# Kernel tuning notes

Measured on AMD Instinct MI355X. Metric: run time of the kernel, lower is better.

## Reference

```python
import jax, jax.numpy as jnp
import numpy as np

EPS = 1e-6


def _mp_cos_pointwise(p, q, M2):
    # p, q: [B, L, K]; M2: [C, K] (squared perspective weights)
    # cosine between (p*M_c) and (q*M_c) along K, per channel c -> [B, L, C]
    num = jnp.einsum('blk,blk,ck->blc', p, q, M2)
    pn = jnp.sqrt(jnp.maximum(jnp.einsum('blk,ck->blc', p * p, M2), EPS))
    qn = jnp.sqrt(jnp.maximum(jnp.einsum('blk,ck->blc', q * q, M2), EPS))
    return num / pn / qn


def setup_inputs() -> dict:
    key = jax.random.key(0)
    ks = jax.random.split(key, 10)
    B, Lq, Ld, K, C = 32, 200, 200, 200, 50
    f32 = jnp.float32
    def unif(k, shape):  # keras 'uniform' init: U(-0.05, 0.05)
        return jax.random.uniform(k, shape, f32, -0.05, 0.05)
    return {
        'q_rep': jax.random.normal(ks[0], (B, Lq, K), f32),
        'q_last': jax.random.normal(ks[1], (B, K), f32),
        'q_mask': jnp.ones((B, Lq), f32),
        'd_rep': jax.random.normal(ks[2], (B, Ld, K), f32),
        'd_last': jax.random.normal(ks[3], (B, K), f32),
        'd_mask': jnp.ones((B, Ld), f32),
        'full_M': unif(ks[4], (C, K)),
        'maxpool_M': unif(ks[5], (C, K)),
        'att_M': unif(ks[6], (C, K)),
        'max_att_M': unif(ks[7], (C, K)),
    }


def reference(q_rep, q_last, q_mask, d_rep, d_last, d_mask,
              full_M, maxpool_M, att_M, max_att_M):
    outputs = []

    # relevancy matrix: cosine(q[b,j,:], d[b,i,:]) -> [B, Ld, Lq]
    num = jnp.einsum('bik,bjk->bij', d_rep, q_rep)
    dn = jnp.sqrt(jnp.maximum(jnp.sum(d_rep * d_rep, -1), EPS))  # [B, Ld]
    qn = jnp.sqrt(jnp.maximum(jnp.sum(q_rep * q_rep, -1), EPS))  # [B, Lq]
    rel = num / qn[:, None, :] / dn[:, :, None]
    rel = rel * q_mask[:, None, :] * d_mask[:, :, None]

    # full matching: cosine(d[b,i]*M_c, q_last[b]*M_c) -> [B, Ld, C]
    M2 = full_M * full_M
    fnum = jnp.einsum('bik,bk,ck->bic', d_rep, q_last, M2)
    fpn = jnp.sqrt(jnp.maximum(jnp.einsum('bik,ck->bic', d_rep * d_rep, M2), EPS))
    fqn = jnp.sqrt(jnp.maximum(jnp.einsum('bk,ck->bc', q_last * q_last, M2), EPS))
    outputs.append(fnum / fpn / fqn[:, None, :])

    # maxpool matching: cosine(d[b,i]*M_c, q[b,j]*M_c) -> [B, Ld, Lq, C]
    M2 = maxpool_M * maxpool_M
    mnum = jnp.einsum('bik,bjk,ck->bijc', d_rep, q_rep, M2)
    mpn = jnp.sqrt(jnp.maximum(jnp.einsum('bik,ck->bic', d_rep * d_rep, M2), EPS))
    mqn = jnp.sqrt(jnp.maximum(jnp.einsum('bjk,ck->bjc', q_rep * q_rep, M2), EPS))
    mm = mnum / mpn[:, :, None, :] / mqn[:, None, :, :]
    outputs.append(jnp.concatenate([jnp.max(mm, axis=2), jnp.mean(mm, axis=2)], axis=2))

    # attentive matching: cosine-weighted q rep (no softmax -> normalize by sum)
    wq = jnp.einsum('bij,bjk->bik', rel, q_rep)
    wq = wq / (jnp.sum(rel, axis=-1) + EPS)[..., None]  # [B, Ld, K]
    outputs.append(_mp_cos_pointwise(d_rep, wq, att_M * att_M))

    # max-attentive matching: gather best-matching q word per d position
    idx = jnp.argmax(rel, axis=2)  # [B, Ld]
    max_q = jnp.take_along_axis(q_rep, idx[:, :, None], axis=1)  # [B, Ld, K]
    outputs.append(_mp_cos_pointwise(d_rep, max_q, max_att_M * max_att_M))

    return jnp.concatenate(outputs, axis=-1)  # [B, Ld, 5*C]
```

## Files before the change

### kernel.cpp

```cpp
#include <hip/hip_runtime.h>
#include <math.h>


#define EPS 1e-6f
#define NEG_HUGE -3.4e38f

typedef __bf16 bf16x8 __attribute__((ext_vector_type(8)));
typedef float f32x16 __attribute__((ext_vector_type(16)));

constexpr size_t OFF_M2ALL = 0;
constexpr size_t OFF_M2B16 = 40000;
constexpr size_t OFF_QB16  = 63296;
constexpr size_t OFF_DB16  = 915264;
constexpr size_t OFF_INVFPN= 1767232;
constexpr size_t OFF_INVMPN= 2087232;
constexpr size_t OFF_INVAPN= 2407232;
constexpr size_t OFF_INVXPN= 2727232;
constexpr size_t OFF_INVMQN= 3047232;
constexpr size_t OFF_INVXQN= 3367232;
constexpr size_t OFF_INVFQN= 3687232;
constexpr size_t OFF_INVDN = 3688832;
constexpr size_t OFF_INVQN = 3695232;
constexpr size_t OFF_IDX   = 3701632;
constexpr size_t OFF_WQ    = 3708032;
constexpr size_t OFF_G     = 4988032;
constexpr size_t OFF_PMAX2 = 6268032;
constexpr size_t OFF_PSUM2 = 6677632;

__global__ __launch_bounds__(256) void k_prep(
    const float* __restrict__ qR, const float* __restrict__ dR,
    const float* __restrict__ fM, const float* __restrict__ mM,
    const float* __restrict__ aM, const float* __restrict__ xM,
    unsigned short* __restrict__ qb16, unsigned short* __restrict__ db16,
    float* __restrict__ invdn, float* __restrict__ invqn,
    float* __restrict__ m2all, unsigned short* __restrict__ m2b16)
{
  int blk = blockIdx.x;
  int tid = threadIdx.x;
  if (blk < 4096) {
    int task = blk*4 + (tid >> 6);
    int l = tid & 63;
    int isQ = task >= 8192;
    int r = isQ ? task - 8192 : task;
    int b = r >> 8, j = r & 255;
    unsigned short* dst = (isQ ? qb16 : db16) + (size_t)r*208;
    if (j < 200) {
      const float* src = (isQ ? qR : dR) + (size_t)(b*200 + j)*200;
      float4 v = {0.f,0.f,0.f,0.f};
      if (l < 50) v = *(const float4*)(src + l*4);
      float s = fmaf(v.x,v.x, fmaf(v.y,v.y, fmaf(v.z,v.z, v.w*v.w)));
#pragma unroll
      for (int m = 32; m; m >>= 1) s += __shfl_xor(s, m);
      if (l == 0) {
        float rr = rsqrtf(fmaxf(s, EPS));
        if (isQ) invqn[b*200 + j] = rr; else invdn[b*200 + j] = rr;
      }
      if (l < 52) {
        ushort4 o = {0,0,0,0};
        if (l < 50) {
          __bf16 h0=(__bf16)v.x, h1=(__bf16)v.y, h2=(__bf16)v.z, h3=(__bf16)v.w;
          o.x = *(unsigned short*)&h0; o.y = *(unsigned short*)&h1;
          o.z = *(unsigned short*)&h2; o.w = *(unsigned short*)&h3;
        }
        *(ushort4*)(dst + l*4) = o;
      }
    } else {
      if (l < 52) { ushort4 z = {0,0,0,0}; *(ushort4*)(dst + l*4) = z; }
    }
  } else {
    int i = (blk - 4096)*256 + tid;
    if (i < 40000) {
      int m = i / 10000, r = i % 10000;
      const float* s = (m==0)?fM:(m==1)?mM:(m==2)?aM:xM;
      float v = s[r];
      m2all[i] = v*v;
    }
    if (i < 224*208) {
      int row = i / 208, k = i % 208;
      unsigned short o = 0;
      if (row < 200 && k < 200) {
        int m = row / 50, c = row % 50;
        const float* s = (m==0)?fM:(m==1)?mM:(m==2)?aM:xM;
        float v = s[c*200 + k];
        __bf16 h = (__bf16)(v*v);
        o = *(unsigned short*)&h;
      }
      m2b16[i] = o;
    }
  }
}

__global__ __launch_bounds__(256,4) void k_gemm1_mfma(
    const float* __restrict__ dR, const float* __restrict__ qR,
    const float* __restrict__ qL, const unsigned short* __restrict__ m2b16,
    float* __restrict__ invfpn, float* __restrict__ invmpn,
    float* __restrict__ invapn, float* __restrict__ invxpn,
    float* __restrict__ invmqn, float* __restrict__ invxqn,
    float* __restrict__ invfqn)
{
  int tid = threadIdx.x;
  int w = tid >> 6, lane = tid & 63;
  int n = lane & 31, h = lane >> 5;
  int task = blockIdx.x*4 + w;
  if (task >= 2807) return;
  int rt = task / 7, nt = task % 7;
  int row = rt*32 + n;

  const float* src;
  if (row < 6400)       src = dR + (size_t)row*200;
  else if (row < 12800) src = qR + (size_t)(row-6400)*200;
  else                  src = qL + (size_t)(row-12800)*200;

  bf16x8 afrag[13];
#pragma unroll
  for (int ks = 0; ks < 13; ks++) {
    int ko = ks*16 + h*8;
    bf16x8 af;
    if (ko < 200) {
      float4 a0 = *(const float4*)(src + ko);
      float4 a1 = *(const float4*)(src + ko + 4);
      af[0] = (__bf16)(a0.x*a0.x); af[1] = (__bf16)(a0.y*a0.y);
      af[2] = (__bf16)(a0.z*a0.z); af[3] = (__bf16)(a0.w*a0.w);
      af[4] = (__bf16)(a1.x*a1.x); af[5] = (__bf16)(a1.y*a1.y);
      af[6] = (__bf16)(a1.z*a1.z); af[7] = (__bf16)(a1.w*a1.w);
    } else {
#pragma unroll
      for (int z = 0; z < 8; z++) af[z] = (__bf16)0.0f;
    }
    afrag[ks] = af;
  }

  f32x16 C;
#pragma unroll
  for (int z = 0; z < 16; z++) C[z] = 0.f;
  const unsigned short* bp = m2b16 + (size_t)(nt*32 + n)*208 + h*8;
#pragma unroll
  for (int ks = 0; ks < 13; ks++) {
    bf16x8 bf = *(const bf16x8*)(bp + ks*16);
    C = __builtin_amdgcn_mfma_f32_32x32x16_bf16(afrag[ks], bf, C, 0, 0, 0);
  }

  int cp = nt*32 + n;
  if (cp < 200) {
    int m = cp / 50, c = cp % 50;
#pragma unroll
    for (int r = 0; r < 16; r++) {
      int grow = rt*32 + (r & 3) + 8*(r >> 2) + 4*h;
      float v = rsqrtf(fmaxf(C[r], EPS));
      if (grow < 6400) {
        if (m == 0)      invfpn[grow*50 + c] = v;
        else if (m == 1) invmpn[grow*50 + c] = v;
        else if (m == 2) invapn[grow*50 + c] = v;
        else             invxpn[grow*50 + c] = v;
      } else if (grow < 12800) {
        int r2 = grow - 6400;
        if (m == 1)      invmqn[c*6400 + r2] = v;
        else if (m == 3) invxqn[r2*50 + c] = v;
      } else {
        if (m == 0)      invfqn[(grow-12800)*50 + c] = v;
      }
    }
  }
}

__global__ __launch_bounds__(256) void k_relwq(
    const float* __restrict__ dR, const float* __restrict__ qR,
    const float* __restrict__ qMask, const float* __restrict__ dMask,
    const float* __restrict__ invdn, const float* __restrict__ invqn,
    float* __restrict__ wq, int* __restrict__ idxout)
{
  __shared__ __align__(16) float qsh[200*68];
  __shared__ float relsh[8][256];
  __shared__ float redv[4][8][2];
  __shared__ int   redi[4][8];
  __shared__ float invrs_sh[8];
  int tid = threadIdx.x;
  int b  = blockIdx.x / 25;
  int i0 = (blockIdx.x % 25) * 8;
  int j = tid, jr = min(j, 199);
  bool jv = j < 200;
  const float* qb = qR + b*40000;
  const float* db = dR + (b*200 + i0)*200;
  float acc[8];
#pragma unroll
  for (int ii = 0; ii < 8; ii++) acc[ii] = 0.f;

  for (int p = 0; p < 4; p++) {
    int kp = p*64; int nk = (p < 3) ? 64 : 8;
    int nch = nk >> 2;
    __syncthreads();
    for (int s = tid; s < 200*nch; s += 256) {
      int jj = s / nch, kk4 = (s - jj*nch)*4;
      float4 v = *(const float4*)(qb + jj*200 + kp + kk4);
      *(float4*)(qsh + jj*68 + kk4) = v;
    }
    __syncthreads();
    for (int k4 = 0; k4 < nk; k4 += 4) {
      float4 qv = *(const float4*)(qsh + jr*68 + k4);
#pragma unroll
      for (int ii = 0; ii < 8; ii++) {
        acc[ii] = fmaf(db[ii*200 + kp + k4 + 0], qv.x, acc[ii]);
        acc[ii] = fmaf(db[ii*200 + kp + k4 + 1], qv.y, acc[ii]);
        acc[ii] = fmaf(db[ii*200 + kp + k4 + 2], qv.z, acc[ii]);
        acc[ii] = fmaf(db[ii*200 + kp + k4 + 3], qv.w, acc[ii]);
      }
    }
  }

  float iqn = invqn[b*200 + jr];
  float qm  = qMask[b*200 + jr];
  int w = tid >> 6, l = tid & 63;
  float rv[8];
#pragma unroll
  for (int ii = 0; ii < 8; ii++) {
    float idn = invdn[b*200 + i0 + ii];
    float dm  = dMask[b*200 + i0 + ii];
    float r = acc[ii]*iqn*idn*qm*dm;
    rv[ii] = r;
    relsh[ii][j] = jv ? r : 0.f;
  }
#pragma unroll
  for (int ii = 0; ii < 8; ii++) {
    float vm = jv ? rv[ii] : NEG_HUGE;
    float vs = jv ? rv[ii] : 0.f;
    int bj = jr;
#pragma unroll
    for (int m = 32; m; m >>= 1) {
      float ov = __shfl_xor(vm, m);
      int   oj = __shfl_xor(bj, m);
      vs += __shfl_xor(vs, m);
      if (ov > vm || (ov == vm && oj < bj)) { vm = ov; bj = oj; }
    }
    if (l == 0) { redv[w][ii][0] = vm; redv[w][ii][1] = vs; redi[w][ii] = bj; }
  }
  __syncthreads();
  if (tid < 8) {
    float bv = redv[0][tid][0], ss = redv[0][tid][1]; int bj = redi[0][tid];
    for (int w2 = 1; w2 < 4; w2++) {
      ss += redv[w2][tid][1];
      float wv = redv[w2][tid][0]; int wj = redi[w2][tid];
      if (wv > bv || (wv == bv && wj < bj)) { bv = wv; bj = wj; }
    }
    invrs_sh[tid] = 1.f/(ss + EPS);
    idxout[b*200 + i0 + tid] = bj;
  }
  __syncthreads();

  int kl = min(tid, 199); bool kv = tid < 200;
  float acw[8];
#pragma unroll
  for (int ii = 0; ii < 8; ii++) acw[ii] = 0.f;
  for (int j0 = 0; j0 < 200; j0 += 4) {
    float qv0 = qb[(j0+0)*200 + kl];
    float qv1 = qb[(j0+1)*200 + kl];
    float qv2 = qb[(j0+2)*200 + kl];
    float qv3 = qb[(j0+3)*200 + kl];
#pragma unroll
    for (int ii = 0; ii < 8; ii++) {
      float4 rs = *(const float4*)&relsh[ii][j0];
      acw[ii] = fmaf(rs.x, qv0, acw[ii]);
      acw[ii] = fmaf(rs.y, qv1, acw[ii]);
      acw[ii] = fmaf(rs.z, qv2, acw[ii]);
      acw[ii] = fmaf(rs.w, qv3, acw[ii]);
    }
  }
#pragma unroll
  for (int ii = 0; ii < 8; ii++) {
    float v = acw[ii]*invrs_sh[ii];
    if (kv) wq[(size_t)(b*200 + i0 + ii)*200 + tid] = v;
  }
}

__global__ __launch_bounds__(256,4) void k_gemm2_mfma(
    const float* __restrict__ dR, const float* __restrict__ qR,
    const float* __restrict__ qL, const float* __restrict__ wq,
    const int* __restrict__ idx, const unsigned short* __restrict__ m2b16,
    float* __restrict__ G)
{
  int tid = threadIdx.x;
  int w = tid >> 6, lane = tid & 63;
  int n = lane & 31, h = lane >> 5;
  int task = blockIdx.x*4 + w;
  int mp = task / 400;
  int sub = task % 400;
  int rt = sub >> 1, nt = sub & 1;
  int row = rt*32 + n;
  int bb = row / 200;
  int msel = (mp == 0) ? 0 : (mp == 3) ? 3 : 2;

  const float* s0 = dR + (size_t)row*200;
  const float* s1;
  if (mp == 0)      s1 = qL + (size_t)bb*200;
  else if (mp == 1) s1 = wq + (size_t)row*200;
  else if (mp == 2) { s0 = wq + (size_t)row*200; s1 = s0; }
  else              s1 = qR + (size_t)(bb*200 + idx[row])*200;

  bf16x8 afrag[13];
#pragma unroll
  for (int ks = 0; ks < 13; ks++) {
    int ko = ks*16 + h*8;
    bf16x8 af;
    if (ko < 200) {
      float4 a0 = *(const float4*)(s0 + ko);
      float4 a1 = *(const float4*)(s0 + ko + 4);
      float4 b0 = *(const float4*)(s1 + ko);
      float4 b1 = *(const float4*)(s1 + ko + 4);
      af[0] = (__bf16)(a0.x*b0.x); af[1] = (__bf16)(a0.y*b0.y);
      af[2] = (__bf16)(a0.z*b0.z); af[3] = (__bf16)(a0.w*b0.w);
      af[4] = (__bf16)(a1.x*b1.x); af[5] = (__bf16)(a1.y*b1.y);
      af[6] = (__bf16)(a1.z*b1.z); af[7] = (__bf16)(a1.w*b1.w);
    } else {
#pragma unroll
      for (int z = 0; z < 8; z++) af[z] = (__bf16)0.0f;
    }
    afrag[ks] = af;
  }

  f32x16 C;
#pragma unroll
  for (int z = 0; z < 16; z++) C[z] = 0.f;
  const unsigned short* bp = m2b16 + (size_t)(msel*50 + nt*32 + n)*208 + h*8;
#pragma unroll
  for (int ks = 0; ks < 13; ks++) {
    bf16x8 bf = *(const bf16x8*)(bp + ks*16);
    C = __builtin_amdgcn_mfma_f32_32x32x16_bf16(afrag[ks], bf, C, 0, 0, 0);
  }
  int cc = nt*32 + n;
  if (cc < 50) {
#pragma unroll
    for (int r = 0; r < 16; r++) {
      int mrow = (r & 3) + 8*(r >> 2) + 4*h;
      G[(size_t)(mp*6400 + rt*32 + mrow)*50 + cc] = C[r];
    }
  }
}

__global__ __launch_bounds__(512,2) void k_maxpool_mfma(
    const unsigned short* __restrict__ db16, const unsigned short* __restrict__ qb16,
    const float* __restrict__ m2all, const float* __restrict__ invmqn,
    float* __restrict__ pmax2, float* __restrict__ psum2)
{
  __shared__ __align__(16) unsigned short qsh[128*216];
  int tid = threadIdx.x;
  int b = blockIdx.x / 50, c = blockIdx.x % 50;
  int w = tid >> 6, lane = tid & 63;
  int n = lane & 31, h = lane >> 5;
  const float* M2 = m2all + 10000 + c*200;
  const unsigned short* dbp = db16 + (size_t)(b*256 + w*32 + n)*208 + h*8;

  bf16x8 afrag[13];
#pragma unroll
  for (int ks = 0; ks < 13; ks++) afrag[ks] = *(const bf16x8*)(dbp + ks*16);

  float vm[16], vs[16];
#pragma unroll
  for (int r = 0; r < 16; r++) { vm[r] = NEG_HUGE; vs[r] = 0.f; }

  for (int jh = 0; jh < 2; jh++) {
    int nrows = jh ? 96 : 128;
    int njt   = jh ? 3 : 4;
    __syncthreads();
    {
      const unsigned short* src = qb16 + (size_t)(b*256 + jh*128)*208;
      const float* iqb = invmqn + c*6400 + b*200;
      for (int s = tid; s < nrows*26; s += 512) {
        int r = s / 26, ch = s - r*26;
        int j = jh*128 + r;
        float iq = (j < 200) ? iqb[j] : 0.f;
        int k0 = ch*8;
        bf16x8 v = *(const bf16x8*)(src + (size_t)r*208 + k0);
        float4 m0 = *(const float4*)(M2 + k0);
        float4 m1 = *(const float4*)(M2 + k0 + 4);
        bf16x8 o;
        o[0] = (__bf16)((float)v[0]*iq*m0.x); o[1] = (__bf16)((float)v[1]*iq*m0.y);
        o[2] = (__bf16)((float)v[2]*iq*m0.z); o[3] = (__bf16)((float)v[3]*iq*m0.w);
        o[4] = (__bf16)((float)v[4]*iq*m1.x); o[5] = (__bf16)((float)v[5]*iq*m1.y);
        o[6] = (__bf16)((float)v[6]*iq*m1.z); o[7] = (__bf16)((float)v[7]*iq*m1.w);
        *(bf16x8*)(qsh + r*216 + k0) = o;
      }
    }
    __syncthreads();

    for (int jt = 0; jt < njt; jt++) {
      f32x16 C;
#pragma unroll
      for (int z = 0; z < 16; z++) C[z] = 0.f;
      const unsigned short* bptr = qsh + (jt*32 + n)*216 + h*8;
#pragma unroll
      for (int ks = 0; ks < 13; ks++) {
        bf16x8 bf = *(const bf16x8*)(bptr + ks*16);
        C = __builtin_amdgcn_mfma_f32_32x32x16_bf16(afrag[ks], bf, C, 0, 0, 0);
      }
      bool jv = (jh*128 + jt*32 + n) < 200;
#pragma unroll
      for (int r = 0; r < 16; r++) {
        vm[r] = fmaxf(vm[r], jv ? C[r] : NEG_HUGE);
        vs[r] += C[r];
      }
    }
  }

#pragma unroll
  for (int r = 0; r < 16; r++) {
    float a = vm[r], s = vs[r];
#pragma unroll
    for (int m = 1; m <= 16; m <<= 1) {
      a = fmaxf(a, __shfl_xor(a, m));
      s += __shfl_xor(s, m);
    }
    vm[r] = a; vs[r] = s;
  }
  if (n == 0) {
#pragma unroll
    for (int r = 0; r < 16; r++) {
      int i = w*32 + (r & 3) + 8*(r >> 2) + 4*h;
      pmax2[(size_t)blockIdx.x*256 + i] = vm[r];
      psum2[(size_t)blockIdx.x*256 + i] = vs[r];
    }
  }
}

__global__ void k_out(
    const float* __restrict__ G, const float* __restrict__ pmax2,
    const float* __restrict__ psum2, const float* __restrict__ invfpn,
    const float* __restrict__ invmpn, const float* __restrict__ invapn,
    const float* __restrict__ invxpn, const float* __restrict__ invfqn,
    const float* __restrict__ invxqn, const int* __restrict__ idx,
    float* __restrict__ out)
{
  int row = blockIdx.x;
  int l = threadIdx.x;
  if (l >= 250) return;
  int b = row / 200, i = row % 200;
  int seg = l / 50, c = l % 50;
  float o;
  if (seg == 0) {
    o = G[(size_t)(0*6400 + row)*50 + c] * invfpn[row*50 + c] * invfqn[b*50 + c];
  } else if (seg == 1) {
    o = pmax2[(size_t)(b*50 + c)*256 + i] * invmpn[row*50 + c];
  } else if (seg == 2) {
    o = psum2[(size_t)(b*50 + c)*256 + i] * invmpn[row*50 + c] * (1.f/200.f);
  } else if (seg == 3) {
    o = G[(size_t)(1*6400 + row)*50 + c] * invapn[row*50 + c]
        * rsqrtf(fmaxf(G[(size_t)(2*6400 + row)*50 + c], EPS));
  } else {
    int jid = idx[row];
    o = G[(size_t)(3*6400 + row)*50 + c] * invxpn[row*50 + c]
        * invxqn[(b*200 + jid)*50 + c];
  }
  out[(size_t)row*250 + l] = o;
}

extern "C" void kernel_launch(void* const* d_in, const int* in_sizes, int n_in,
                              void* d_out, int out_size, void* d_ws, size_t ws_size,
                              hipStream_t stream) {
  const float* qR = (const float*)d_in[0];
  const float* qL = (const float*)d_in[1];
  const float* qM = (const float*)d_in[2];
  const float* dR = (const float*)d_in[3];
  const float* dM = (const float*)d_in[5];
  const float* fullM = (const float*)d_in[6];
  const float* mpM   = (const float*)d_in[7];
  const float* attM  = (const float*)d_in[8];
  const float* xM    = (const float*)d_in[9];

  float* ws  = (float*)d_ws;
  float* out = (float*)d_out;

  float* m2all  = ws + OFF_M2ALL;
  unsigned short* m2b16 = (unsigned short*)(ws + OFF_M2B16);
  unsigned short* qb16 = (unsigned short*)(ws + OFF_QB16);
  unsigned short* db16 = (unsigned short*)(ws + OFF_DB16);
  float* invfpn = ws + OFF_INVFPN;
  float* invmpn = ws + OFF_INVMPN;
  float* invapn = ws + OFF_INVAPN;
  float* invxpn = ws + OFF_INVXPN;
  float* invmqn = ws + OFF_INVMQN;
  float* invxqn = ws + OFF_INVXQN;
  float* invfqn = ws + OFF_INVFQN;
  float* invdn  = ws + OFF_INVDN;
  float* invqn  = ws + OFF_INVQN;
  int*   idxp   = (int*)(ws + OFF_IDX);
  float* wqp    = ws + OFF_WQ;
  float* G      = ws + OFF_G;
  float* pmax2  = ws + OFF_PMAX2;
  float* psum2  = ws + OFF_PSUM2;

  k_prep<<<4278, 256, 0, stream>>>(qR, dR, fullM, mpM, attM, xM,
                                   qb16, db16, invdn, invqn, m2all, m2b16);
  k_gemm1_mfma<<<702, 256, 0, stream>>>(dR, qR, qL, m2b16,
                                        invfpn, invmpn, invapn, invxpn,
                                        invmqn, invxqn, invfqn);
  k_relwq<<<800, 256, 0, stream>>>(dR, qR, qM, dM, invdn, invqn, wqp, idxp);
  k_gemm2_mfma<<<400, 256, 0, stream>>>(dR, qR, qL, wqp, idxp, m2b16, G);
  k_maxpool_mfma<<<1600, 512, 0, stream>>>(db16, qb16, m2all, invmqn, pmax2, psum2);
  k_out<<<6400, 256, 0, stream>>>(G, pmax2, psum2, invfpn, invmpn, invapn,
                                  invxpn, invfqn, invxqn, idxp, out);
}
```

Baseline: 278.3 us.

## Merge independent kernels into two horizontally fused launches, drop LDS staging in relwq

The norm GEMM and the relevancy/weighted-q kernel become one launch, with blocks dispatched by block index. The maxpool MFMA and the per-row GEMM2 become a second launch. This removes two kernel launches and their tail gaps, and lets independent work overlap on the GPU. The relwq part now reads q rows straight from global memory instead of staging them through shared memory. GEMM2 tasks now run 8 waves per 512-thread block instead of 4 per 256. In exchange, the fused kernels share a launch bound and a register budget, which may lower occupancy for the lighter branch.

```diff
diff --git a/kernel.cpp b/kernel.cpp
--- a/kernel.cpp
+++ b/kernel.cpp
@@ -90,188 +90,178 @@
   }
 }
 
-__global__ __launch_bounds__(256,4) void k_gemm1_mfma(
+__global__ __launch_bounds__(256) void k_mid(
     const float* __restrict__ dR, const float* __restrict__ qR,
     const float* __restrict__ qL, const unsigned short* __restrict__ m2b16,
     float* __restrict__ invfpn, float* __restrict__ invmpn,
     float* __restrict__ invapn, float* __restrict__ invxpn,
     float* __restrict__ invmqn, float* __restrict__ invxqn,
-    float* __restrict__ invfqn)
-{
-  int tid = threadIdx.x;
-  int w = tid >> 6, lane = tid & 63;
-  int n = lane & 31, h = lane >> 5;
-  int task = blockIdx.x*4 + w;
-  if (task >= 2807) return;
-  int rt = task / 7, nt = task % 7;
-  int row = rt*32 + n;
-
-  const float* src;
-  if (row < 6400)       src = dR + (size_t)row*200;
-  else if (row < 12800) src = qR + (size_t)(row-6400)*200;
-  else                  src = qL + (size_t)(row-12800)*200;
-
-  bf16x8 afrag[13];
-#pragma unroll
-  for (int ks = 0; ks < 13; ks++) {
-    int ko = ks*16 + h*8;
-    bf16x8 af;
-    if (ko < 200) {
-      float4 a0 = *(const float4*)(src + ko);
-      float4 a1 = *(const float4*)(src + ko + 4);
-      af[0] = (__bf16)(a0.x*a0.x); af[1] = (__bf16)(a0.y*a0.y);
-      af[2] = (__bf16)(a0.z*a0.z); af[3] = (__bf16)(a0.w*a0.w);
-      af[4] = (__bf16)(a1.x*a1.x); af[5] = (__bf16)(a1.y*a1.y);
-      af[6] = (__bf16)(a1.z*a1.z); af[7] = (__bf16)(a1.w*a1.w);
-    } else {
-#pragma unroll
-      for (int z = 0; z < 8; z++) af[z] = (__bf16)0.0f;
-    }
-    afrag[ks] = af;
-  }
-
-  f32x16 C;
-#pragma unroll
-  for (int z = 0; z < 16; z++) C[z] = 0.f;
-  const unsigned short* bp = m2b16 + (size_t)(nt*32 + n)*208 + h*8;
-#pragma unroll
-  for (int ks = 0; ks < 13; ks++) {
-    bf16x8 bf = *(const bf16x8*)(bp + ks*16);
-    C = __builtin_amdgcn_mfma_f32_32x32x16_bf16(afrag[ks], bf, C, 0, 0, 0);
-  }
-
-  int cp = nt*32 + n;
-  if (cp < 200) {
-    int m = cp / 50, c = cp % 50;
-#pragma unroll
-    for (int r = 0; r < 16; r++) {
-      int grow = rt*32 + (r & 3) + 8*(r >> 2) + 4*h;
-      float v = rsqrtf(fmaxf(C[r], EPS));
-      if (grow < 6400) {
-        if (m == 0)      invfpn[grow*50 + c] = v;
-        else if (m == 1) invmpn[grow*50 + c] = v;
-        else if (m == 2) invapn[grow*50 + c] = v;
-        else             invxpn[grow*50 + c] = v;
-      } else if (grow < 12800) {
-        int r2 = grow - 6400;
-        if (m == 1)      invmqn[c*6400 + r2] = v;
-        else if (m == 3) invxqn[r2*50 + c] = v;
-      } else {
-        if (m == 0)      invfqn[(grow-12800)*50 + c] = v;
-      }
-    }
-  }
-}
-
-__global__ __launch_bounds__(256) void k_relwq(
-    const float* __restrict__ dR, const float* __restrict__ qR,
+    float* __restrict__ invfqn,
     const float* __restrict__ qMask, const float* __restrict__ dMask,
     const float* __restrict__ invdn, const float* __restrict__ invqn,
     float* __restrict__ wq, int* __restrict__ idxout)
 {
-  __shared__ __align__(16) float qsh[200*68];
-  __shared__ float relsh[8][256];
-  __shared__ float redv[4][8][2];
-  __shared__ int   redi[4][8];
-  __shared__ float invrs_sh[8];
   int tid = threadIdx.x;
-  int b  = blockIdx.x / 25;
-  int i0 = (blockIdx.x % 25) * 8;
-  int j = tid, jr = min(j, 199);
-  bool jv = j < 200;
-  const float* qb = qR + b*40000;
-  const float* db = dR + (b*200 + i0)*200;
-  float acc[8];
-#pragma unroll
-  for (int ii = 0; ii < 8; ii++) acc[ii] = 0.f;
-
-  for (int p = 0; p < 4; p++) {
-    int kp = p*64; int nk = (p < 3) ? 64 : 8;
-    int nch = nk >> 2;
+  if (blockIdx.x < 702) {
+    int w = tid >> 6, lane = tid & 63;
+    int n = lane & 31, h = lane >> 5;
+    int task = blockIdx.x*4 + w;
+    if (task >= 2807) return;
+    int rt = task / 7, nt = task % 7;
+    int row = rt*32 + n;
+
+    const float* src;
+    if (row < 6400)       src = dR + (size_t)row*200;
+    else if (row < 12800) src = qR + (size_t)(row-6400)*200;
+    else                  src = qL + (size_t)(row-12800)*200;
+
+    bf16x8 afrag[13];
+#pragma unroll
+    for (int ks = 0; ks < 13; ks++) {
+      int ko = ks*16 + h*8;
+      bf16x8 af;
+      if (ko < 200) {
+        float4 a0 = *(const float4*)(src + ko);
+        float4 a1 = *(const float4*)(src + ko + 4);
+        af[0] = (__bf16)(a0.x*a0.x); af[1] = (__bf16)(a0.y*a0.y);
+        af[2] = (__bf16)(a0.z*a0.z); af[3] = (__bf16)(a0.w*a0.w);
+        af[4] = (__bf16)(a1.x*a1.x); af[5] = (__bf16)(a1.y*a1.y);
+        af[6] = (__bf16)(a1.z*a1.z); af[7] = (__bf16)(a1.w*a1.w);
+      } else {
+#pragma unroll
+        for (int z = 0; z < 8; z++) af[z] = (__bf16)0.0f;
+      }
+      afrag[ks] = af;
+    }
+
+    f32x16 C;
+#pragma unroll
+    for (int z = 0; z < 16; z++) C[z] = 0.f;
+    const unsigned short* bp = m2b16 + (size_t)(nt*32 + n)*208 + h*8;
+#pragma unroll
+    for (int ks = 0; ks < 13; ks++) {
+      bf16x8 bf = *(const bf16x8*)(bp + ks*16);
+      C = __builtin_amdgcn_mfma_f32_32x32x16_bf16(afrag[ks], bf, C, 0, 0, 0);
+    }
+
+    int cp = nt*32 + n;
+    if (cp < 200) {
+      int m = cp / 50, c = cp % 50;
+#pragma unroll
+      for (int r = 0; r < 16; r++) {
+        int grow = rt*32 + (r & 3) + 8*(r >> 2) + 4*h;
+        float v = rsqrtf(fmaxf(C[r], EPS));
+        if (grow < 6400) {
+          if (m == 0)      invfpn[grow*50 + c] = v;
+          else if (m == 1) invmpn[grow*50 + c] = v;
+          else if (m == 2) invapn[grow*50 + c] = v;
+          else             invxpn[grow*50 + c] = v;
+        } else if (grow < 12800) {
+          int r2 = grow - 6400;
+          if (m == 1)      invmqn[c*6400 + r2] = v;
+          else if (m == 3) invxqn[r2*50 + c] = v;
+        } else {
+          if (m == 0)      invfqn[(grow-12800)*50 + c] = v;
+        }
+      }
+    }
+  } else {
+    __shared__ float relsh[8][256];
+    __shared__ float redv[4][8][2];
+    __shared__ int   redi[4][8];
+    __shared__ float invrs_sh[8];
+    int blk = blockIdx.x - 702;
+    int b  = blk / 25;
+    int i0 = (blk % 25) * 8;
+    int j = tid, jr = min(j, 199);
+    bool jv = j < 200;
+    const float* qb = qR + b*40000;
+    const float* db = dR + (b*200 + i0)*200;
+    float acc[8];
+#pragma unroll
+    for (int ii = 0; ii < 8; ii++) acc[ii] = 0.f;
+
+    const float* qrow = qb + jr*200;
+    for (int k4 = 0; k4 < 200; k4 += 4) {
+      float4 qv = *(const float4*)(qrow + k4);
+#pragma unroll
+      for (int ii = 0; ii < 8; ii++) {
+        acc[ii] = fmaf(db[ii*200 + k4 + 0], qv.x, acc[ii]);
+        acc[ii] = fmaf(db[ii*200 + k4 + 1], qv.y, acc[ii]);
+        acc[ii] = fmaf(db[ii*200 + k4 + 2], qv.z, acc[ii]);
+        acc[ii] = fmaf(db[ii*200 + k4 + 3], qv.w, acc[ii]);
+      }
+    }
+
+    float iqn = invqn[b*200 + jr];
+    float qm  = qMask[b*200 + jr];
+    int w = tid >> 6, l = tid & 63;
+    float rv[8];
+#pragma unroll
+    for (int ii = 0; ii < 8; ii++) {
+      float idn = invdn[b*200 + i0 + ii];
+      float dm  = dMask[b*200 + i0 + ii];
+      float r = acc[ii]*iqn*idn*qm*dm;
+      rv[ii] = r;
+      relsh[ii][j] = jv ? r : 0.f;
+    }
+#pragma unroll
+    for (int ii = 0; ii < 8; ii++) {
+      float vm = jv ? rv[ii] : NEG_HUGE;
+      float vs = jv ? rv[ii] : 0.f;
+      int bj = jr;
+#pragma unroll
+      for (int m = 32; m; m >>= 1) {
+        float ov = __shfl_xor(vm, m);
+        int   oj = __shfl_xor(bj, m);
+        vs += __shfl_xor(vs, m);
+        if (ov > vm || (ov == vm && oj < bj)) { vm = ov; bj = oj; }
+      }
+      if (l == 0) { redv[w][ii][0] = vm; redv[w][ii][1] = vs; redi[w][ii] = bj; }
+    }
     __syncthreads();
-    for (int s = tid; s < 200*nch; s += 256) {
-      int jj = s / nch, kk4 = (s - jj*nch)*4;
-      float4 v = *(const float4*)(qb + jj*200 + kp + kk4);
-      *(float4*)(qsh + jj*68 + kk4) = v;
+    if (tid < 8) {
+      float bv = redv[0][tid][0], ss = redv[0][tid][1]; int bj = redi[0][tid];
+      for (int w2 = 1; w2 < 4; w2++) {
+        ss += redv[w2][tid][1];
+        float wv = redv[w2][tid][0]; int wj = redi[w2][tid];
+        if (wv > bv || (wv == bv && wj < bj)) { bv = wv; bj = wj; }
+      }
+      invrs_sh[tid] = 1.f/(ss + EPS);
+      idxout[b*200 + i0 + tid] = bj;
     }
     __syncthreads();
-    for (int k4 = 0; k4 < nk; k4 += 4) {
-      float4 qv = *(const float4*)(qsh + jr*68 + k4);
+
+    int kl = min(tid, 199); bool kv = tid < 200;
+    float acw[8];
+#pragma unroll
+    for (int ii = 0; ii < 8; ii++) acw[ii] = 0.f;
+    for (int j0 = 0; j0 < 200; j0 += 4) {
+      float qv0 = qb[(j0+0)*200 + kl];
+      float qv1 = qb[(j0+1)*200 + kl];
+      float qv2 = qb[(j0+2)*200 + kl];
+      float qv3 = qb[(j0+3)*200 + kl];
 #pragma unroll
       for (int ii = 0; ii < 8; ii++) {
-        acc[ii] = fmaf(db[ii*200 + kp + k4 + 0], qv.x, acc[ii]);
-        acc[ii] = fmaf(db[ii*200 + kp + k4 + 1], qv.y, acc[ii]);
-        acc[ii] = fmaf(db[ii*200 + kp + k4 + 2], qv.z, acc[ii]);
-        acc[ii] = fmaf(db[ii*200 + kp + k4 + 3], qv.w, acc[ii]);
-      }
-    }
-  }
-
-  float iqn = invqn[b*200 + jr];
-  float qm  = qMask[b*200 + jr];
-  int w = tid >> 6, l = tid & 63;
-  float rv[8];
-#pragma unroll
-  for (int ii = 0; ii < 8; ii++) {
-    float idn = invdn[b*200 + i0 + ii];
-    float dm  = dMask[b*200 + i0 + ii];
-    float r = acc[ii]*iqn*idn*qm*dm;
-    rv[ii] = r;
-    relsh[ii][j] = jv ? r : 0.f;
-  }
-#pragma unroll
-  for (int ii = 0; ii < 8; ii++) {
-    float vm = jv ? rv[ii] : NEG_HUGE;
-    float vs = jv ? rv[ii] : 0.f;
-    int bj = jr;
-#pragma unroll
-    for (int m = 32; m; m >>= 1) {
-      float ov = __shfl_xor(vm, m);
-      int   oj = __shfl_xor(bj, m);
-      vs += __shfl_xor(vs, m);
-      if (ov > vm || (ov == vm && oj < bj)) { vm = ov; bj = oj; }
-    }
-    if (l == 0) { redv[w][ii][0] = vm; redv[w][ii][1] = vs; redi[w][ii] = bj; }
-  }
-  __syncthreads();
-  if (tid < 8) {
-    float bv = redv[0][tid][0], ss = redv[0][tid][1]; int bj = redi[0][tid];
-    for (int w2 = 1; w2 < 4; w2++) {
-      ss += redv[w2][tid][1];
-      float wv = redv[w2][tid][0]; int wj = redi[w2][tid];
-      if (wv > bv || (wv == bv && wj < bj)) { bv = wv; bj = wj; }
-    }
-    invrs_sh[tid] = 1.f/(ss + EPS);
-    idxout[b*200 + i0 + tid] = bj;
-  }
-  __syncthreads();
-
-  int kl = min(tid, 199); bool kv = tid < 200;
-  float acw[8];
-#pragma unroll
-  for (int ii = 0; ii < 8; ii++) acw[ii] = 0.f;
-  for (int j0 = 0; j0 < 200; j0 += 4) {
-    float qv0 = qb[(j0+0)*200 + kl];
-    float qv1 = qb[(j0+1)*200 + kl];
-    float qv2 = qb[(j0+2)*200 + kl];
-    float qv3 = qb[(j0+3)*200 + kl];
+        float4 rs = *(const float4*)&relsh[ii][j0];
+        acw[ii] = fmaf(rs.x, qv0, acw[ii]);
+        acw[ii] = fmaf(rs.y, qv1, acw[ii]);
+        acw[ii] = fmaf(rs.z, qv2, acw[ii]);
+        acw[ii] = fmaf(rs.w, qv3, acw[ii]);
+      }
+    }
 #pragma unroll
     for (int ii = 0; ii < 8; ii++) {
-      float4 rs = *(const float4*)&relsh[ii][j0];
-      acw[ii] = fmaf(rs.x, qv0, acw[ii]);
-      acw[ii] = fmaf(rs.y, qv1, acw[ii]);
-      acw[ii] = fmaf(rs.z, qv2, acw[ii]);
-      acw[ii] = fmaf(rs.w, qv3, acw[ii]);
-    }
-  }
-#pragma unroll
-  for (int ii = 0; ii < 8; ii++) {
-    float v = acw[ii]*invrs_sh[ii];
-    if (kv) wq[(size_t)(b*200 + i0 + ii)*200 + tid] = v;
+      float v = acw[ii]*invrs_sh[ii];
+      if (kv) wq[(size_t)(b*200 + i0 + ii)*200 + tid] = v;
+    }
   }
 }
 
-__global__ __launch_bounds__(256,4) void k_gemm2_mfma(
+__global__ __launch_bounds__(512,2) void k_big(
+    const unsigned short* __restrict__ db16, const unsigned short* __restrict__ qb16,
+    const float* __restrict__ m2all, const float* __restrict__ invmqn,
+    float* __restrict__ pmax2, float* __restrict__ psum2,
     const float* __restrict__ dR, const float* __restrict__ qR,
     const float* __restrict__ qL, const float* __restrict__ wq,
     const int* __restrict__ idx, const unsigned short* __restrict__ m2b16,
@@ -280,142 +270,135 @@
   int tid = threadIdx.x;
   int w = tid >> 6, lane = tid & 63;
   int n = lane & 31, h = lane >> 5;
-  int task = blockIdx.x*4 + w;
-  int mp = task / 400;
-  int sub = task % 400;
-  int rt = sub >> 1, nt = sub & 1;
-  int row = rt*32 + n;
-  int bb = row / 200;
-  int msel = (mp == 0) ? 0 : (mp == 3) ? 3 : 2;
-
-  const float* s0 = dR + (size_t)row*200;
-  const float* s1;
-  if (mp == 0)      s1 = qL + (size_t)bb*200;
-  else if (mp == 1) s1 = wq + (size_t)row*200;
-  else if (mp == 2) { s0 = wq + (size_t)row*200; s1 = s0; }
-  else              s1 = qR + (size_t)(bb*200 + idx[row])*200;
-
-  bf16x8 afrag[13];
-#pragma unroll
-  for (int ks = 0; ks < 13; ks++) {
-    int ko = ks*16 + h*8;
-    bf16x8 af;
-    if (ko < 200) {
-      float4 a0 = *(const float4*)(s0 + ko);
-      float4 a1 = *(const float4*)(s0 + ko + 4);
-      float4 b0 = *(const float4*)(s1 + ko);
-      float4 b1 = *(const float4*)(s1 + ko + 4);
-      af[0] = (__bf16)(a0.x*b0.x); af[1] = (__bf16)(a0.y*b0.y);
-      af[2] = (__bf16)(a0.z*b0.z); af[3] = (__bf16)(a0.w*b0.w);
-      af[4] = (__bf16)(a1.x*b1.x); af[5] = (__bf16)(a1.y*b1.y);
-      af[6] = (__bf16)(a1.z*b1.z); af[7] = (__bf16)(a1.w*b1.w);
-    } else {
-#pragma unroll
-      for (int z = 0; z < 8; z++) af[z] = (__bf16)0.0f;
-    }
-    afrag[ks] = af;
-  }
-
-  f32x16 C;
-#pragma unroll
-  for (int z = 0; z < 16; z++) C[z] = 0.f;
-  const unsigned short* bp = m2b16 + (size_t)(msel*50 + nt*32 + n)*208 + h*8;
-#pragma unroll
-  for (int ks = 0; ks < 13; ks++) {
-    bf16x8 bf = *(const bf16x8*)(bp + ks*16);
-    C = __builtin_amdgcn_mfma_f32_32x32x16_bf16(afrag[ks], bf, C, 0, 0, 0);
-  }
-  int cc = nt*32 + n;
-  if (cc < 50) {
+  if (blockIdx.x < 1600) {
+    __shared__ __align__(16) unsigned short qsh[128*216];
+    int b = blockIdx.x / 50, c = blockIdx.x % 50;
+    const float* M2 = m2all + 10000 + c*200;
+    const unsigned short* dbp = db16 + (size_t)(b*256 + w*32 + n)*208 + h*8;
+
+    bf16x8 afrag[13];
+#pragma unroll
+    for (int ks = 0; ks < 13; ks++) afrag[ks] = *(const bf16x8*)(dbp + ks*16);
+
+    float vm[16], vs[16];
+#pragma unroll
+    for (int r = 0; r < 16; r++) { vm[r] = NEG_HUGE; vs[r] = 0.f; }
+
+    for (int jh = 0; jh < 2; jh++) {
+      int nrows = jh ? 96 : 128;
+      int njt   = jh ? 3 : 4;
+      __syncthreads();
+      {
+        const unsigned short* src = qb16 + (size_t)(b*256 + jh*128)*208;
+        const float* iqb = invmqn + c*6400 + b*200;
+        for (int s = tid; s < nrows*26; s += 512) {
+          int r = s / 26, ch = s - r*26;
+          int j = jh*128 + r;
+          float iq = (j < 200) ? iqb[j] : 0.f;
+          int k0 = ch*8;
+          bf16x8 v = *(const bf16x8*)(src + (size_t)r*208 + k0);
+          float4 m0 = *(const float4*)(M2 + k0);
+          float4 m1 = *(const float4*)(M2 + k0 + 4);
+          bf16x8 o;
+          o[0] = (__bf16)((float)v[0]*iq*m0.x); o[1] = (__bf16)((float)v[1]*iq*m0.y);
+          o[2] = (__bf16)((float)v[2]*iq*m0.z); o[3] = (__bf16)((float)v[3]*iq*m0.w);
+          o[4] = (__bf16)((float)v[4]*iq*m1.x); o[5] = (__bf16)((float)v[5]*iq*m1.y);
+          o[6] = (__bf16)((float)v[6]*iq*m1.z); o[7] = (__bf16)((float)v[7]*iq*m1.w);
+          *(bf16x8*)(qsh + r*216 + k0) = o;
+        }
+      }
+      __syncthreads();
+
+      for (int jt = 0; jt < njt; jt++) {
+        f32x16 C;
+#pragma unroll
+        for (int z = 0; z < 16; z++) C[z] = 0.f;
+        const unsigned short* bptr = qsh + (jt*32 + n)*216 + h*8;
+#pragma unroll
+        for (int ks = 0; ks < 13; ks++) {
+          bf16x8 bf = *(const bf16x8*)(bptr + ks*16);
+          C = __builtin_amdgcn_mfma_f32_32x32x16_bf16(afrag[ks], bf, C, 0, 0, 0);
+        }
+        bool jv = (jh*128 + jt*32 + n) < 200;
+#pragma unroll
+        for (int r = 0; r < 16; r++) {
+          vm[r] = fmaxf(vm[r], jv ? C[r] : NEG_HUGE);
+          vs[r] += C[r];
+        }
+      }
+    }
+
 #pragma unroll
     for (int r = 0; r < 16; r++) {
-      int mrow = (r & 3) + 8*(r >> 2) + 4*h;
-      G[(size_t)(mp*6400 + rt*32 + mrow)*50 + cc] = C[r];
-    }
-  }
-}
-
-__global__ __launch_bounds__(512,2) void k_maxpool_mfma(
-    const unsigned short* __restrict__ db16, const unsigned short* __restrict__ qb16,
-    const float* __restrict__ m2all, const float* __restrict__ invmqn,
-    float* __restrict__ pmax2, float* __restrict__ psum2)
-{
-  __shared__ __align__(16) unsigned short qsh[128*216];
-  int tid = threadIdx.x;
-  int b = blockIdx.x / 50, c = blockIdx.x % 50;
-  int w = tid >> 6, lane = tid & 63;
-  int n = lane & 31, h = lane >> 5;
-  const float* M2 = m2all + 10000 + c*200;
-  const unsigned short* dbp = db16 + (size_t)(b*256 + w*32 + n)*208 + h*8;
-
-  bf16x8 afrag[13];
-#pragma unroll
-  for (int ks = 0; ks < 13; ks++) afrag[ks] = *(const bf16x8*)(dbp + ks*16);
-
-  float vm[16], vs[16];
-#pragma unroll
-  for (int r = 0; r < 16; r++) { vm[r] = NEG_HUGE; vs[r] = 0.f; }
-
-  for (int jh = 0; jh < 2; jh++) {
-    int nrows = jh ? 96 : 128;
-    int njt   = jh ? 3 : 4;
-    __syncthreads();
-    {
-      const unsigned short* src = qb16 + (size_t)(b*256 + jh*128)*208;
-      const float* iqb = invmqn + c*6400 + b*200;
-      for (int s = tid; s < nrows*26; s += 512) {
-        int r = s / 26, ch = s - r*26;
-        int j = jh*128 + r;
-        float iq = (j < 200) ? iqb[j] : 0.f;
-        int k0 = ch*8;
-        bf16x8 v = *(const bf16x8*)(src + (size_t)r*208 + k0);
-        float4 m0 = *(const float4*)(M2 + k0);
-        float4 m1 = *(const float4*)(M2 + k0 + 4);
-        bf16x8 o;
-        o[0] = (__bf16)((float)v[0]*iq*m0.x); o[1] = (__bf16)((float)v[1]*iq*m0.y);
-        o[2] = (__bf16)((float)v[2]*iq*m0.z); o[3] = (__bf16)((float)v[3]*iq*m0.w);
-        o[4] = (__bf16)((float)v[4]*iq*m1.x); o[5] = (__bf16)((float)v[5]*iq*m1.y);
-        o[6] = (__bf16)((float)v[6]*iq*m1.z); o[7] = (__bf16)((float)v[7]*iq*m1.w);
-        *(bf16x8*)(qsh + r*216 + k0) = o;
-      }
-    }
-    __syncthreads();
-
-    for (int jt = 0; jt < njt; jt++) {
-      f32x16 C;
-#pragma unroll
-      for (int z = 0; z < 16; z++) C[z] = 0.f;
-      const unsigned short* bptr = qsh + (jt*32 + n)*216 + h*8;
-#pragma unroll
-      for (int ks = 0; ks < 13; ks++) {
-        bf16x8 bf = *(const bf16x8*)(bptr + ks*16);
-        C = __builtin_amdgcn_mfma_f32_32x32x16_bf16(afrag[ks], bf, C, 0, 0, 0);
-      }
-      bool jv = (jh*128 + jt*32 + n) < 200;
+      float a = vm[r], s = vs[r];
+#pragma unroll
+      for (int m = 1; m <= 16; m <<= 1) {
+        a = fmaxf(a, __shfl_xor(a, m));
+        s += __shfl_xor(s, m);
+      }
+      vm[r] = a; vs[r] = s;
+    }
+    if (n == 0) {
 #pragma unroll
       for (int r = 0; r < 16; r++) {
-        vm[r] = fmaxf(vm[r], jv ? C[r] : NEG_HUGE);
-        vs[r] += C[r];
-      }
-    }
-  }
-
-#pragma unroll
-  for (int r = 0; r < 16; r++) {
-    float a = vm[r], s = vs[r];
-#pragma unroll
-    for (int m = 1; m <= 16; m <<= 1) {
-      a = fmaxf(a, __shfl_xor(a, m));
-      s += __shfl_xor(s, m);
-    }
-    vm[r] = a; vs[r] = s;
-  }
-  if (n == 0) {
-#pragma unroll
-    for (int r = 0; r < 16; r++) {
-      int i = w*32 + (r & 3) + 8*(r >> 2) + 4*h;
-      pmax2[(size_t)blockIdx.x*256 + i] = vm[r];
-      psum2[(size_t)blockIdx.x*256 + i] = vs[r];
+        int i = w*32 + (r & 3) + 8*(r >> 2) + 4*h;
+        pmax2[(size_t)blockIdx.x*256 + i] = vm[r];
+        psum2[(size_t)blockIdx.x*256 + i] = vs[r];
+      }
+    }
+  } else {
+    int task = (blockIdx.x - 1600)*8 + w;
+    int mp = task / 400;
+    int sub = task % 400;
+    int rt = sub >> 1, nt = sub & 1;
+    int row = rt*32 + n;
+    int bb = row / 200;
+    int msel = (mp == 0) ? 0 : (mp == 3) ? 3 : 2;
+
+    const float* s0 = dR + (size_t)row*200;
+    const float* s1;
+    if (mp == 0)      s1 = qL + (size_t)bb*200;
+    else if (mp == 1) s1 = wq + (size_t)row*200;
+    else if (mp == 2) { s0 = wq + (size_t)row*200; s1 = s0; }
+    else              s1 = qR + (size_t)(bb*200 + idx[row])*200;
+
+    bf16x8 afrag[13];
+#pragma unroll
+    for (int ks = 0; ks < 13; ks++) {
+      int ko = ks*16 + h*8;
+      bf16x8 af;
+      if (ko < 200) {
+        float4 a0 = *(const float4*)(s0 + ko);
+        float4 a1 = *(const float4*)(s0 + ko + 4);
+        float4 b0 = *(const float4*)(s1 + ko);
+        float4 b1 = *(const float4*)(s1 + ko + 4);
+        af[0] = (__bf16)(a0.x*b0.x); af[1] = (__bf16)(a0.y*b0.y);
+        af[2] = (__bf16)(a0.z*b0.z); af[3] = (__bf16)(a0.w*b0.w);
+        af[4] = (__bf16)(a1.x*b1.x); af[5] = (__bf16)(a1.y*b1.y);
+        af[6] = (__bf16)(a1.z*b1.z); af[7] = (__bf16)(a1.w*b1.w);
+      } else {
+#pragma unroll
+        for (int z = 0; z < 8; z++) af[z] = (__bf16)0.0f;
+      }
+      afrag[ks] = af;
+    }
+
+    f32x16 C;
+#pragma unroll
+    for (int z = 0; z < 16; z++) C[z] = 0.f;
+    const unsigned short* bp = m2b16 + (size_t)(msel*50 + nt*32 + n)*208 + h*8;
+#pragma unroll
+    for (int ks = 0; ks < 13; ks++) {
+      bf16x8 bf = *(const bf16x8*)(bp + ks*16);
+      C = __builtin_amdgcn_mfma_f32_32x32x16_bf16(afrag[ks], bf, C, 0, 0, 0);
+    }
+    int cc = nt*32 + n;
+    if (cc < 50) {
+#pragma unroll
+      for (int r = 0; r < 16; r++) {
+        int mrow = (r & 3) + 8*(r >> 2) + 4*h;
+        G[(size_t)(mp*6400 + rt*32 + mrow)*50 + cc] = C[r];
+      }
     }
   }
 }
@@ -488,12 +471,12 @@
 
   k_prep<<<4278, 256, 0, stream>>>(qR, dR, fullM, mpM, attM, xM,
                                    qb16, db16, invdn, invqn, m2all, m2b16);
-  k_gemm1_mfma<<<702, 256, 0, stream>>>(dR, qR, qL, m2b16,
-                                        invfpn, invmpn, invapn, invxpn,
-                                        invmqn, invxqn, invfqn);
-  k_relwq<<<800, 256, 0, stream>>>(dR, qR, qM, dM, invdn, invqn, wqp, idxp);
-  k_gemm2_mfma<<<400, 256, 0, stream>>>(dR, qR, qL, wqp, idxp, m2b16, G);
-  k_maxpool_mfma<<<1600, 512, 0, stream>>>(db16, qb16, m2all, invmqn, pmax2, psum2);
+  k_mid<<<1502, 256, 0, stream>>>(dR, qR, qL, m2b16,
+                                  invfpn, invmpn, invapn, invxpn,
+                                  invmqn, invxqn, invfqn,
+                                  qM, dM, invdn, invqn, wqp, idxp);
+  k_big<<<1800, 512, 0, stream>>>(db16, qb16, m2all, invmqn, pmax2, psum2,
+                                  dR, qR, qL, wqp, idxp, m2b16, G);
   k_out<<<6400, 256, 0, stream>>>(G, pmax2, psum2, invfpn, invmpn, invapn,
                                   invxpn, invfqn, invxqn, idxp, out);
 }
```

After: 248.1 us. 1.12x faster.
